# Optimization experiments

Hardware: AMD Instinct MI355X
Metric: run time of the kernel (lower is better)

The kernel has to match this reference:

```python
import jax, jax.numpy as jnp
import numpy as np

BS, IN_F, OUT_F = 1024, 128, 100000
M, S, ALPHA = 0.35, 30.0, 0.5


def _l2norm(x):
    # F.normalize: x / max(||x||, eps)
    n = jnp.sqrt(jnp.sum(x * x, axis=-1, keepdims=True))
    return x / jnp.maximum(n, 1e-12)


def setup_inputs() -> dict:
    key = jax.random.key(0)
    k1, k2, k3 = jax.random.split(key, 3)
    return {
        "input": jax.random.normal(k1, (BS, IN_F), dtype=jnp.float32),
        "label": jax.random.randint(k2, (BS,), 0, OUT_F, dtype=jnp.int64),
        "weight": jax.random.normal(k3, (OUT_F, IN_F), dtype=jnp.float32),
    }


def reference(input, label, weight):
    wn = _l2norm(weight)                      # [nc, d]
    fn = _l2norm(input)                       # [bs, d]
    logits = jnp.einsum('bd,cd->bc', fn, wn)  # [bs, nc] cosine sims
    bs = fn.shape[0]
    rows = jnp.arange(bs)

    pos = jnp.take_along_axis(logits, label[:, None], axis=1)[:, 0] * S  # [bs]
    # negatives: all classes except the label (replaces masked_select + view)
    neg = (logits * S).at[rows, label].set(-jnp.inf)
    lse_neg = jax.nn.logsumexp(neg, axis=1)   # [bs]

    # loss = mean(log(1 + exp(m + lse_neg - pos)))
    loss = jnp.mean(jax.nn.softplus(M + lse_neg - pos))

    # weight.data update: per-class mean of normalized features for classes
    # present in the batch (the torch loop is exactly a segment-mean; note
    # weight_update aliases weight.data so the final blend is a no-op and the
    # result is simply: present rows <- class mean, other rows unchanged).
    sums = jax.ops.segment_sum(fn, label, num_segments=OUT_F)                # [nc, d]
    counts = jax.ops.segment_sum(jnp.ones((bs,), fn.dtype), label, num_segments=OUT_F)
    present = counts > 0
    class_mean = sums / jnp.maximum(counts, 1.0)[:, None]
    new_weight = jnp.where(present[:, None], class_mean, weight)

    return loss, new_weight
```

## Files before the change

### kernel.cpp

```cpp
#include <hip/hip_runtime.h>

#define BS 1024
#define D 128
#define NC 100000
#define NCP 100096
#define NTILES 782
#define S_SCALE 30.0f
#define MARGIN 0.35f
#define S2LOG2E 43.2808512f

typedef __attribute__((ext_vector_type(8))) short bf16x8;
typedef __attribute__((ext_vector_type(4))) float f32x4;

__device__ __forceinline__ unsigned short f2bf(float f) {
    union { float f; unsigned u; } x; x.f = f;
    unsigned u = x.u;
    u += 0x7FFFu + ((u >> 16) & 1u);
    return (unsigned short)(u >> 16);
}


__global__ void prep_fn(const float* __restrict__ inp, const int* __restrict__ label,
                        const float* __restrict__ wt,
                        float* __restrict__ fn_f32, unsigned short* __restrict__ fn_fr,
                        float* __restrict__ counts, float* __restrict__ pos) {
    int row = blockIdx.x * 4 + (threadIdx.x >> 6);
    int lane = threadIdx.x & 63;
    float2 v = *(const float2*)(inp + row * D + lane * 2);
    float s = v.x * v.x + v.y * v.y;
    #pragma unroll
    for (int m = 1; m < 64; m <<= 1) s += __shfl_xor(s, m);
    float inv = 1.0f / fmaxf(sqrtf(s), 1e-12f);
    float a = v.x * inv, b = v.y * inv;
    *(float2*)(fn_f32 + row * D + lane * 2) = make_float2(a, b);
    unsigned pack = (unsigned)f2bf(a) | ((unsigned)f2bf(b) << 16);
    ((unsigned*)fn_fr)[(row >> 4) * 1024 + (lane >> 2) * 64 + ((row & 15) << 2) + (lane & 3)] = pack;

    int c = label[row];
    float2 wv = *(const float2*)(wt + c * D + lane * 2);
    float sw_ = wv.x * wv.x + wv.y * wv.y;
    float dt  = wv.x * a + wv.y * b;
    #pragma unroll
    for (int m = 1; m < 64; m <<= 1) { sw_ += __shfl_xor(sw_, m); dt += __shfl_xor(dt, m); }
    if (lane == 0) {
        float invw = 1.0f / fmaxf(sqrtf(sw_), 1e-12f);
        pos[row] = S_SCALE * dt * invw;
        atomicAdd(counts + c, 1.0f);
    }
}

__global__ void prep_wn(const float* __restrict__ wt, const float* __restrict__ counts,
                        unsigned short* __restrict__ wn_fr, float* __restrict__ outw) {
    int wv = threadIdx.x >> 6, lane = threadIdx.x & 63;
    int row = blockIdx.x * 4 + wv;
    unsigned* dst = (unsigned*)wn_fr + (row >> 4) * 1024 + (lane >> 2) * 64 +
                    ((row & 15) << 2) + (lane & 3);
    if (row < NC) {
        float2 v = *(const float2*)(wt + row * D + lane * 2);
        float s = v.x * v.x + v.y * v.y;
        #pragma unroll
        for (int m = 1; m < 64; m <<= 1) s += __shfl_xor(s, m);
        float inv = 1.0f / fmaxf(sqrtf(s), 1e-12f);
        *dst = (unsigned)f2bf(v.x * inv) | ((unsigned)f2bf(v.y * inv) << 16);
        float cnt = counts[row];
        float2 o = (cnt > 0.0f) ? make_float2(0.0f, 0.0f) : v;
        *(float2*)(outw + row * D + lane * 2) = o;
    } else {
        *dst = 0u;
    }
}

__global__ __launch_bounds__(256, 3) void main_gemm(
    const unsigned short* __restrict__ fnfr, const unsigned short* __restrict__ wnfr,
    float* __restrict__ sumexp) {
    __shared__ float red[1024];
    int tid = threadIdx.x;
    int lane = tid & 63, w = tid >> 6;
    int l15 = lane & 15;
    int cls_half = w >> 1;
    int bat_half = w & 1;

    #pragma unroll
    for (int i = 0; i < 4; i++) red[tid + i * 256] = 0.0f;

    bf16x8 af[4][4];
    {
        const char* gA = (const char*)wnfr + (size_t)blockIdx.x * 32768 +
                         cls_half * 16384 + lane * 16;
        #pragma unroll
        for (int mt = 0; mt < 4; mt++)
            #pragma unroll
            for (int ks = 0; ks < 4; ks++)
                af[ks][mt] = *(const bf16x8*)(gA + mt * 4096 + ks * 1024);
    }

    __syncthreads();

    const char* gB = (const char*)fnfr + bat_half * 8192 + lane * 16;

    bf16x8 b[2][4];
    #pragma unroll
    for (int nt = 0; nt < 2; nt++)
        #pragma unroll
        for (int ks = 0; ks < 4; ks++)
            b[nt][ks] = *(const bf16x8*)(gB + nt * 4096 + ks * 1024);

    for (int c = 0; c < 16; c++) {
        f32x4 acc[4][2];
        #pragma unroll
        for (int mt = 0; mt < 4; mt++)
            #pragma unroll
            for (int nt = 0; nt < 2; nt++)
                acc[mt][nt] = (f32x4){0.0f, 0.0f, 0.0f, 0.0f};

        #pragma unroll
        for (int ks = 0; ks < 4; ks++)
            #pragma unroll
            for (int mt = 0; mt < 4; mt++)
                #pragma unroll
                for (int nt = 0; nt < 2; nt++)
                    acc[mt][nt] = __builtin_amdgcn_mfma_f32_16x16x32_bf16(
                        af[ks][mt], b[nt][ks], acc[mt][nt], 0, 0, 0);

        if (c < 15) {
            const char* gBn = gB + (c + 1) * 16384;
            #pragma unroll
            for (int nt = 0; nt < 2; nt++)
                #pragma unroll
                for (int ks = 0; ks < 4; ks++)
                    b[nt][ks] = *(const bf16x8*)(gBn + nt * 4096 + ks * 1024);
        }

        float s0 = 0.0f, s1 = 0.0f;
        #pragma unroll
        for (int mt = 0; mt < 4; mt++)
            #pragma unroll
            for (int r = 0; r < 4; r++) {
                s0 += __builtin_amdgcn_exp2f(fmaf(acc[mt][0][r], S2LOG2E, -S2LOG2E));
                s1 += __builtin_amdgcn_exp2f(fmaf(acc[mt][1][r], S2LOG2E, -S2LOG2E));
            }
        s0 += __shfl_xor(s0, 16); s0 += __shfl_xor(s0, 32);
        s1 += __shfl_xor(s1, 16); s1 += __shfl_xor(s1, 32);
        if (lane < 16) {
            int base = c * 64 + bat_half * 32 + l15;
            atomicAdd(&red[base], s0);
            atomicAdd(&red[base + 16], s1);
        }
    }

    __syncthreads();
    #pragma unroll
    for (int i = 0; i < 4; i++) {
        int idx = tid + i * 256;
        atomicAdd(sumexp + idx, red[idx]);
    }
}

__global__ void loss_k(const float* __restrict__ sumexp, const float* __restrict__ pos,
                       float* __restrict__ out) {
    __shared__ float red[256];
    int t = threadIdx.x;
    float acc = 0.0f;
    #pragma unroll
    for (int i = 0; i < 4; i++) {
        int r = t + i * 256;
        float p = pos[r];
        float sneg = fmaxf(sumexp[r] - __expf(p - 30.0f), 1e-38f);
        float lse = 30.0f + logf(sneg);
        float z = MARGIN + lse - p;
        acc += fmaxf(z, 0.0f) + log1pf(__expf(-fabsf(z)));
    }
    red[t] = acc;
    __syncthreads();
    for (int s = 128; s > 0; s >>= 1) {
        if (t < s) red[t] += red[t + s];
        __syncthreads();
    }
    if (t == 0) out[0] = red[0] * (1.0f / 1024.0f);
}

__global__ void addmean_k(const float* __restrict__ fn_f32, const int* __restrict__ label,
                          const float* __restrict__ counts, float* __restrict__ outw) {
    int b = blockIdx.x, t = threadIdx.x;
    int c = label[b];
    float cnt = counts[c];
    atomicAdd(outw + c * D + t, fn_f32[b * D + t] / cnt);
}

extern "C" void kernel_launch(void* const* d_in, const int* in_sizes, int n_in,
                              void* d_out, int out_size, void* d_ws, size_t ws_size,
                              hipStream_t stream) {
    (void)in_sizes; (void)n_in; (void)out_size; (void)ws_size;
    const float* inp   = (const float*)d_in[0];
    const int*   label = (const int*)d_in[1];
    const float* wt    = (const float*)d_in[2];
    float* out = (float*)d_out;

    char* w = (char*)d_ws;
    float*          fn_f32 = (float*)(w);
    unsigned short* fn_fr  = (unsigned short*)(w + 524288);
    unsigned short* wn_fr  = (unsigned short*)(w + 786432);
    float*          sumexp = (float*)(w + 26411008);
    float*          counts = (float*)(w + 26415104);
    float*          pos    = (float*)(w + 26815104);

    hipMemsetAsync(w + 26411008, 0, 404096, stream);

    prep_fn<<<BS / 4, 256, 0, stream>>>(inp, label, wt, fn_f32, fn_fr, counts, pos);
    prep_wn<<<NCP / 4, 256, 0, stream>>>(wt, counts, wn_fr, out + 1);
    main_gemm<<<NTILES, 256, 0, stream>>>(fn_fr, wn_fr, sumexp);
    addmean_k<<<BS, D, 0, stream>>>(fn_f32, label, counts, out + 1);
    loss_k<<<1, 256, 0, stream>>>(sumexp, pos, out);
}
```

Before: 169.3 us.

## Restructure main GEMM to keep batch in registers and stream weights via LDS

The main GEMM now keeps the batch features resident in registers, 32 rows per wave across 16 waves per block. It streams 64-class weight tiles into double-buffered LDS with global_load_lds, in a persistent grid of 256x2 blocks. Previously each block held the weight tile in registers and re-read the whole batch from global memory. The aim is to cut redundant reads of the batch features and the per-chunk shared-memory atomics, accumulating per-thread partial sums and doing one global atomic at the end. In exchange there is a block-wide barrier per tile and much larger 1024-thread blocks, which may limit occupancy or leave some CUs with uneven work.

Result: faster. 160.3 us (-5.3%).

```diff
diff --git a/kernel.cpp b/kernel.cpp
--- a/kernel.cpp
+++ b/kernel.cpp
@@ -4,7 +4,8 @@
 #define D 128
 #define NC 100000
 #define NCP 100096
-#define NTILES 782
+#define NT64 1564
+#define PHASES 256
 #define S_SCALE 30.0f
 #define MARGIN 0.35f
 #define S2LOG2E 43.2808512f
@@ -17,6 +18,12 @@
     unsigned u = x.u;
     u += 0x7FFFu + ((u >> 16) & 1u);
     return (unsigned short)(u >> 16);
+}
+
+__device__ __forceinline__ void gld_lds16(const void* g, void* l) {
+    auto gp = (const __attribute__((address_space(1))) unsigned int*)(g);
+    auto lp = (__attribute__((address_space(3))) unsigned int*)(l);
+    __builtin_amdgcn_global_load_lds(gp, lp, 16, 0, 0);
 }
 
 
@@ -70,89 +77,89 @@
     }
 }
 
-__global__ __launch_bounds__(256, 3) void main_gemm(
+__global__ __launch_bounds__(1024, 4) void main_gemm(
     const unsigned short* __restrict__ fnfr, const unsigned short* __restrict__ wnfr,
     float* __restrict__ sumexp) {
-    __shared__ float red[1024];
+    __shared__ __align__(16) short Ws[2][8192];
     int tid = threadIdx.x;
     int lane = tid & 63, w = tid >> 6;
-    int l15 = lane & 15;
-    int cls_half = w >> 1;
-    int bat_half = w & 1;
-
-    #pragma unroll
-    for (int i = 0; i < 4; i++) red[tid + i * 256] = 0.0f;
-
-    bf16x8 af[4][4];
+    int half = blockIdx.y;
+    int rb0 = half * 32 + w * 2;
+
+    bf16x8 bf[2][4];
     {
-        const char* gA = (const char*)wnfr + (size_t)blockIdx.x * 32768 +
-                         cls_half * 16384 + lane * 16;
-        #pragma unroll
-        for (int mt = 0; mt < 4; mt++)
+        const char* gB = (const char*)fnfr + (size_t)rb0 * 4096 + lane * 16;
+        #pragma unroll
+        for (int cg = 0; cg < 2; cg++)
             #pragma unroll
             for (int ks = 0; ks < 4; ks++)
-                af[ks][mt] = *(const bf16x8*)(gA + mt * 4096 + ks * 1024);
-    }
-
+                bf[cg][ks] = *(const bf16x8*)(gB + cg * 4096 + ks * 1024);
+    }
+    #pragma unroll
+    for (int cg = 0; cg < 2; cg++)
+        #pragma unroll
+        for (int ks = 0; ks < 4; ks++)
+            asm volatile("" : "+v"(bf[cg][ks]));
+
+    float sums[2] = {0.0f, 0.0f};
+
+    int t0 = blockIdx.x;
+    {
+        const char* g = (const char*)wnfr + (size_t)t0 * 16384 + w * 1024 + lane * 16;
+        gld_lds16(g, (char*)Ws[0] + w * 1024);
+    }
     __syncthreads();
 
-    const char* gB = (const char*)fnfr + bat_half * 8192 + lane * 16;
-
-    bf16x8 b[2][4];
-    #pragma unroll
-    for (int nt = 0; nt < 2; nt++)
-        #pragma unroll
-        for (int ks = 0; ks < 4; ks++)
-            b[nt][ks] = *(const bf16x8*)(gB + nt * 4096 + ks * 1024);
-
-    for (int c = 0; c < 16; c++) {
+    int cur = 0;
+    for (int t = t0; t < NT64; t += PHASES) {
+        int nxt = t + PHASES;
+        if (nxt < NT64) {
+            const char* g = (const char*)wnfr + (size_t)nxt * 16384 + w * 1024 + lane * 16;
+            gld_lds16(g, (char*)Ws[cur ^ 1] + w * 1024);
+        }
+
         f32x4 acc[4][2];
         #pragma unroll
-        for (int mt = 0; mt < 4; mt++)
-            #pragma unroll
-            for (int nt = 0; nt < 2; nt++)
-                acc[mt][nt] = (f32x4){0.0f, 0.0f, 0.0f, 0.0f};
-
-        #pragma unroll
-        for (int ks = 0; ks < 4; ks++)
-            #pragma unroll
-            for (int mt = 0; mt < 4; mt++)
+        for (int ag = 0; ag < 4; ag++)
+            #pragma unroll
+            for (int cg = 0; cg < 2; cg++)
+                acc[ag][cg] = (f32x4){0.0f, 0.0f, 0.0f, 0.0f};
+
+        const char* W = (const char*)Ws[cur];
+        #pragma unroll
+        for (int ks = 0; ks < 4; ks++) {
+            bf16x8 a[4];
+            #pragma unroll
+            for (int ag = 0; ag < 4; ag++)
+                a[ag] = *(const bf16x8*)(W + ag * 4096 + ks * 1024 + lane * 16);
+            #pragma unroll
+            for (int ag = 0; ag < 4; ag++)
                 #pragma unroll
-                for (int nt = 0; nt < 2; nt++)
-                    acc[mt][nt] = __builtin_amdgcn_mfma_f32_16x16x32_bf16(
-                        af[ks][mt], b[nt][ks], acc[mt][nt], 0, 0, 0);
-
-        if (c < 15) {
-            const char* gBn = gB + (c + 1) * 16384;
-            #pragma unroll
-            for (int nt = 0; nt < 2; nt++)
+                for (int cg = 0; cg < 2; cg++)
+                    acc[ag][cg] = __builtin_amdgcn_mfma_f32_16x16x32_bf16(
+                        a[ag], bf[cg][ks], acc[ag][cg], 0, 0, 0);
+        }
+
+        #pragma unroll
+        for (int ag = 0; ag < 4; ag++)
+            #pragma unroll
+            for (int cg = 0; cg < 2; cg++)
                 #pragma unroll
-                for (int ks = 0; ks < 4; ks++)
-                    b[nt][ks] = *(const bf16x8*)(gBn + nt * 4096 + ks * 1024);
-        }
-
-        float s0 = 0.0f, s1 = 0.0f;
-        #pragma unroll
-        for (int mt = 0; mt < 4; mt++)
-            #pragma unroll
-            for (int r = 0; r < 4; r++) {
-                s0 += __builtin_amdgcn_exp2f(fmaf(acc[mt][0][r], S2LOG2E, -S2LOG2E));
-                s1 += __builtin_amdgcn_exp2f(fmaf(acc[mt][1][r], S2LOG2E, -S2LOG2E));
-            }
-        s0 += __shfl_xor(s0, 16); s0 += __shfl_xor(s0, 32);
-        s1 += __shfl_xor(s1, 16); s1 += __shfl_xor(s1, 32);
-        if (lane < 16) {
-            int base = c * 64 + bat_half * 32 + l15;
-            atomicAdd(&red[base], s0);
-            atomicAdd(&red[base + 16], s1);
-        }
-    }
-
-    __syncthreads();
-    #pragma unroll
-    for (int i = 0; i < 4; i++) {
-        int idx = tid + i * 256;
-        atomicAdd(sumexp + idx, red[idx]);
+                for (int r = 0; r < 4; r++)
+                    sums[cg] += __builtin_amdgcn_exp2f(
+                        fmaf(acc[ag][cg][r], S2LOG2E, -S2LOG2E));
+
+        __syncthreads();
+        cur ^= 1;
+    }
+
+    #pragma unroll
+    for (int cg = 0; cg < 2; cg++) {
+        float s = sums[cg];
+        s += __shfl_xor(s, 16);
+        s += __shfl_xor(s, 32);
+        if (lane < 16)
+            atomicAdd(sumexp + half * 512 + w * 32 + cg * 16 + lane, s);
     }
 }
 
@@ -208,7 +215,7 @@
 
     prep_fn<<<BS / 4, 256, 0, stream>>>(inp, label, wt, fn_f32, fn_fr, counts, pos);
     prep_wn<<<NCP / 4, 256, 0, stream>>>(wt, counts, wn_fr, out + 1);
-    main_gemm<<<NTILES, 256, 0, stream>>>(fn_fr, wn_fr, sumexp);
+    main_gemm<<<dim3(PHASES, 2), 1024, 0, stream>>>(fn_fr, wn_fr, sumexp);
     addmean_k<<<BS, D, 0, stream>>>(fn_f32, label, counts, out + 1);
     loss_k<<<1, 256, 0, stream>>>(sumexp, pos, out);
 }
```
